# Kernel optimization log

Measured on AMD Instinct MI355X. Metric: run time of the kernel, lower is better.

Reference implementation:

```python
import jax, jax.numpy as jnp
import numpy as np

B, N_IN, N_MF, N_RULES, N_OUT_MEM, N_OUT = 16384, 6, 5, 2048, 12, 2
TANH_CENTERS = np.array([0.0, 0.75], dtype=np.float32)
TANH_SCALE = np.array([4.0, 0.75], dtype=np.float32)
EPS = 1e-12


def setup_inputs() -> dict:
    key = jax.random.key(0)
    k = jax.random.split(key, 6)
    x = jax.random.normal(k[0], (B, N_IN), dtype=jnp.float32)
    mf_centers = jax.random.normal(k[1], (N_IN, N_MF), dtype=jnp.float32)
    # strictly positive widths for the Gaussian memberships
    mf_scales = jax.random.uniform(k[2], (N_IN, N_MF), dtype=jnp.float32) + 0.5
    out_centers = jax.random.normal(k[3], (N_OUT_MEM,), dtype=jnp.float32)
    input_rules = jax.random.randint(k[4], (N_RULES, N_IN), 0, N_IN * N_MF, dtype=jnp.int32)
    output_rules = jax.random.randint(k[5], (N_RULES, N_OUT), 0, N_OUT_MEM, dtype=jnp.int32)
    return {"x": x, "mf_centers": mf_centers, "mf_scales": mf_scales,
            "out_centers": out_centers, "input_rules": input_rules,
            "output_rules": output_rules}


def reference(x, mf_centers, mf_scales, out_centers, input_rules, output_rules):
    # fuzzify: Gaussian membership per (input var, MF) -> [B, N_IN*N_MF]
    z = (x[:, :, None] - mf_centers[None]) / mf_scales[None]      # [B, N_IN, N_MF]
    fuzzified = jnp.exp(-z * z).reshape(x.shape[0], -1)           # [B, 30]
    # rules: gather antecedent memberships, min t-norm over antecedents
    gathered = fuzzified[:, input_rules]                          # [B, R, N_IN]
    weights = jnp.min(gathered, axis=2)                           # [B, R]
    # L1 normalize across rules (F.normalize p=1, dim=1)
    l1 = jnp.sum(jnp.abs(weights), axis=1, keepdims=True)
    normalized = weights / jnp.maximum(l1, EPS)
    # defuzzify: gather output-membership centers per rule, then matmul
    ow = out_centers[output_rules]                                # [R, N_OUT]
    defuzz = normalized @ ow                                      # [B, N_OUT]
    # constrain scaling
    return jnp.tanh(defuzz) * jnp.asarray(TANH_SCALE) + jnp.asarray(TANH_CENTERS)
```

## Files before the change

### kernel.cpp

```cpp
#include <hip/hip_runtime.h>
#include <hip/hip_bf16.h>

#define BATCH      16384
#define N_IN       6
#define N_MF       5
#define N_FUZZ     30
#define N_RULES    2048

#define ROWS_PER_BLOCK 64
#define BLOCK_THREADS  1024
#define WAVES          (BLOCK_THREADS / 64)
#define RULES_PER_WAVE (N_RULES / WAVES)

__global__ __launch_bounds__(BLOCK_THREADS, 1)
void anfis_kernel(const void* __restrict__ x_,
                  const void* __restrict__ mfc_,
                  const void* __restrict__ mfs_,
                  const void* __restrict__ oc_,
                  const int*  __restrict__ input_rules,
                  const int*  __restrict__ output_rules,
                  void* __restrict__ out_) {
    __shared__ float        fuzz[N_FUZZ][ROWS_PER_BLOCK];
    __shared__ float        p_l1[WAVES][ROWS_PER_BLOCK];
    __shared__ float        p_d0[WAVES][ROWS_PER_BLOCK];
    __shared__ float        p_d1[WAVES][ROWS_PER_BLOCK];
    __shared__ unsigned int packed_lds[N_RULES];
    __shared__ float2       ow_lds[N_RULES];
    __shared__ int          dtype_flag;

    const int t    = threadIdx.x;
    const int row0 = blockIdx.x * ROWS_PER_BLOCK;

    if (t == 0) {
        const unsigned int* w = (const unsigned int*)mfs_;
        int ok = 1;
        for (int k = 0; k < 15; ++k) {
            const unsigned int v = w[k];
            const float lo = __uint_as_float(v << 16);
            const float hi = __uint_as_float(v & 0xffff0000u);
            if (!(lo >= 0.4f && lo <= 1.6f && hi >= 0.4f && hi <= 1.6f)) { ok = 0; break; }
        }
        dtype_flag = ok;
    }
    __syncthreads();
    const bool is_bf16 = (dtype_flag != 0);

    for (int r = t; r < N_RULES; r += BLOCK_THREADS) {
        const int* rp = input_rules + r * N_IN;
        unsigned int p = 0;
#pragma unroll
        for (int i = 0; i < N_IN; ++i) {
            p |= ((unsigned int)rp[i] & 31u) << (5 * i);
        }
        packed_lds[r] = p;
        const int o0i = output_rules[2 * r + 0];
        const int o1i = output_rules[2 * r + 1];
        float o0, o1;
        if (is_bf16) {
            const unsigned short* oc = (const unsigned short*)oc_;
            o0 = __uint_as_float((unsigned int)oc[o0i] << 16);
            o1 = __uint_as_float((unsigned int)oc[o1i] << 16);
        } else {
            const float* oc = (const float*)oc_;
            o0 = oc[o0i];
            o1 = oc[o1i];
        }
        ow_lds[r] = make_float2(o0, o1);
    }

    for (int idx = t; idx < N_FUZZ * ROWS_PER_BLOCK; idx += BLOCK_THREADS) {
        const int v   = idx >> 6;
        const int row = idx & 63;
        const int i   = v / N_MF;
        float xv, c, s;
        if (is_bf16) {
            const unsigned short* xp = (const unsigned short*)x_;
            const unsigned short* cp = (const unsigned short*)mfc_;
            const unsigned short* sp = (const unsigned short*)mfs_;
            xv = __uint_as_float((unsigned int)xp[(row0 + row) * N_IN + i] << 16);
            c  = __uint_as_float((unsigned int)cp[v] << 16);
            s  = __uint_as_float((unsigned int)sp[v] << 16);
        } else {
            xv = ((const float*)x_)[(row0 + row) * N_IN + i];
            c  = ((const float*)mfc_)[v];
            s  = ((const float*)mfs_)[v];
        }
        const float z = (xv - c) / s;
        fuzz[v][row] = __expf(-z * z);
    }
    __syncthreads();

    const int lane = t & 63;
    const int wave = __builtin_amdgcn_readfirstlane(t >> 6);

    float acc_l1 = 0.0f, acc_d0 = 0.0f, acc_d1 = 0.0f;
    const int rbase = wave * RULES_PER_WAVE;
#pragma unroll 4
    for (int j = 0; j < RULES_PER_WAVE; ++j) {
        const int r = rbase + j;
        const unsigned int p = packed_lds[r];
        const float2 o = ow_lds[r];
        float w = fuzz[p & 31u][lane];
        w = fminf(w, fuzz[(p >> 5)  & 31u][lane]);
        w = fminf(w, fuzz[(p >> 10) & 31u][lane]);
        w = fminf(w, fuzz[(p >> 15) & 31u][lane]);
        w = fminf(w, fuzz[(p >> 20) & 31u][lane]);
        w = fminf(w, fuzz[(p >> 25) & 31u][lane]);
        acc_l1 += w;
        acc_d0 += w * o.x;
        acc_d1 += w * o.y;
    }
    p_l1[wave][lane] = acc_l1;
    p_d0[wave][lane] = acc_d0;
    p_d1[wave][lane] = acc_d1;
    __syncthreads();

    if (t < ROWS_PER_BLOCK) {
        float l1 = 0.0f, d0 = 0.0f, d1 = 0.0f;
#pragma unroll
        for (int wv = 0; wv < WAVES; ++wv) {
            l1 += p_l1[wv][t];
            d0 += p_d0[wv][t];
            d1 += p_d1[wv][t];
        }
        const float inv = 1.0f / fmaxf(l1, 1e-12f);
        const float y0 = tanhf(d0 * inv) * 4.00f + 0.00f;
        const float y1 = tanhf(d1 * inv) * 0.75f + 0.75f;
        if (is_bf16) {
            __hip_bfloat162 o;
            o.x = __float2bfloat16(y0);
            o.y = __float2bfloat16(y1);
            ((__hip_bfloat162*)out_)[row0 + t] = o;
        } else {
            ((float2*)out_)[row0 + t] = make_float2(y0, y1);
        }
    }
}

extern "C" void kernel_launch(void* const* d_in, const int* in_sizes, int n_in,
                              void* d_out, int out_size, void* d_ws, size_t ws_size,
                              hipStream_t stream) {
    (void)d_ws; (void)ws_size; (void)in_sizes; (void)n_in; (void)out_size;
    anfis_kernel<<<BATCH / ROWS_PER_BLOCK, BLOCK_THREADS, 0, stream>>>(
        d_in[0], d_in[1], d_in[2], d_in[3],
        (const int*)d_in[4], (const int*)d_in[5],
        d_out);
}
```

Before: 86.86 us.

## Split into prep/main/finalize kernels with fp16 packed memberships and rule splitting

Moves rule packing and output-center gathering into a separate prep kernel writing to workspace, so main blocks no longer redo it per block. The main kernel handles 256 rows per block using fp16 packed membership values (4 rows per lane via two packed-half min chains), reads rule data from global/cache, and splits rules across 4 blocks, writing partial sums that a finalize kernel reduces and applies tanh. This cuts per-block setup and LDS gather count, at the cost of two extra launches, a workspace round-trip, and fp16 rounding of membership values before the min.

Result: faster. 80.96 us (-6.8%).

```diff
diff --git a/kernel.cpp b/kernel.cpp
--- a/kernel.cpp
+++ b/kernel.cpp
@@ -6,143 +6,242 @@
 #define N_MF       5
 #define N_FUZZ     30
 #define N_RULES    2048
-
-#define ROWS_PER_BLOCK 64
-#define BLOCK_THREADS  1024
-#define WAVES          (BLOCK_THREADS / 64)
-#define RULES_PER_WAVE (N_RULES / WAVES)
-
-__global__ __launch_bounds__(BLOCK_THREADS, 1)
-void anfis_kernel(const void* __restrict__ x_,
-                  const void* __restrict__ mfc_,
-                  const void* __restrict__ mfs_,
-                  const void* __restrict__ oc_,
-                  const int*  __restrict__ input_rules,
-                  const int*  __restrict__ output_rules,
-                  void* __restrict__ out_) {
-    __shared__ float        fuzz[N_FUZZ][ROWS_PER_BLOCK];
-    __shared__ float        p_l1[WAVES][ROWS_PER_BLOCK];
-    __shared__ float        p_d0[WAVES][ROWS_PER_BLOCK];
-    __shared__ float        p_d1[WAVES][ROWS_PER_BLOCK];
-    __shared__ unsigned int packed_lds[N_RULES];
-    __shared__ float2       ow_lds[N_RULES];
-    __shared__ int          dtype_flag;
-
-    const int t    = threadIdx.x;
-    const int row0 = blockIdx.x * ROWS_PER_BLOCK;
-
-    if (t == 0) {
-        const unsigned int* w = (const unsigned int*)mfs_;
-        int ok = 1;
-        for (int k = 0; k < 15; ++k) {
-            const unsigned int v = w[k];
-            const float lo = __uint_as_float(v << 16);
-            const float hi = __uint_as_float(v & 0xffff0000u);
-            if (!(lo >= 0.4f && lo <= 1.6f && hi >= 0.4f && hi <= 1.6f)) { ok = 0; break; }
+#define N_OUT_MEM  12
+
+#define ROWS_PB    256
+#define SPLITS     4
+#define RULES_PB   (N_RULES / SPLITS)
+#define THREADS    1024
+#define WAVES      16
+#define RULES_PW   (RULES_PB / WAVES)
+#define ROWGROUPS  (BATCH / ROWS_PB)
+
+#define WS_PACKED_OFF  0
+#define WS_OW_OFF      8192
+#define WS_PART_OFF    24576
+
+typedef _Float16 f16x2 __attribute__((ext_vector_type(2)));
+
+__device__ inline int probe_is_bf16(const void* mfs) {
+    const unsigned int* w = (const unsigned int*)mfs;
+    int ok = 1;
+    for (int k = 0; k < 15; ++k) {
+        const unsigned int v = w[k];
+        const float lo = __uint_as_float(v << 16);
+        const float hi = __uint_as_float(v & 0xffff0000u);
+        if (!(lo >= 0.4f && lo <= 1.6f && hi >= 0.4f && hi <= 1.6f)) { ok = 0; break; }
+    }
+    return ok;
+}
+
+__global__ void anfis_prep(const int* __restrict__ input_rules,
+                           const int* __restrict__ output_rules,
+                           const void* __restrict__ oc_,
+                           const void* __restrict__ mfs_,
+                           unsigned int* __restrict__ packed,
+                           float2* __restrict__ ow) {
+    __shared__ int flag;
+    if (threadIdx.x == 0) flag = probe_is_bf16(mfs_);
+    __syncthreads();
+    const bool is_bf16 = (flag != 0);
+
+    const int r = blockIdx.x * blockDim.x + threadIdx.x;
+    if (r >= N_RULES) return;
+    const int* rp = input_rules + r * N_IN;
+    unsigned int p = 0;
+#pragma unroll
+    for (int i = 0; i < N_IN; ++i) p |= ((unsigned int)rp[i] & 31u) << (5 * i);
+    packed[r] = p;
+
+    const int o0i = output_rules[2 * r + 0];
+    const int o1i = output_rules[2 * r + 1];
+    float o0, o1;
+    if (is_bf16) {
+        const unsigned short* oc = (const unsigned short*)oc_;
+        o0 = __uint_as_float((unsigned int)oc[o0i] << 16);
+        o1 = __uint_as_float((unsigned int)oc[o1i] << 16);
+    } else {
+        const float* oc = (const float*)oc_;
+        o0 = oc[o0i]; o1 = oc[o1i];
+    }
+    ow[r] = make_float2(o0, o1);
+}
+
+__global__ __launch_bounds__(THREADS, 4)
+void anfis_main(const void* __restrict__ x_,
+                const void* __restrict__ mfc_,
+                const void* __restrict__ mfs_,
+                const unsigned int* __restrict__ packed,
+                const float2* __restrict__ ow,
+                float* __restrict__ partials) {
+    __shared__ float xs[ROWS_PB * N_IN];
+    __shared__ float2 cinv[N_FUZZ];
+    __shared__ uint2 fuzz4[N_FUZZ][64];
+    __shared__ float pl1[WAVES][ROWS_PB];
+    __shared__ float pd0[WAVES][ROWS_PB];
+    __shared__ float pd1[WAVES][ROWS_PB];
+    __shared__ int flag;
+
+    const int t     = threadIdx.x;
+    const int g     = blockIdx.x >> 2;
+    const int split = blockIdx.x & 3;
+    const int row0  = g * ROWS_PB;
+
+    if (t == 0) flag = probe_is_bf16(mfs_);
+    __syncthreads();
+    const bool is_bf16 = (flag != 0);
+
+    if (is_bf16) {
+        const unsigned short* xp = (const unsigned short*)x_ + row0 * N_IN;
+        for (int i = t; i < ROWS_PB * N_IN; i += THREADS)
+            xs[i] = __uint_as_float((unsigned int)xp[i] << 16);
+    } else {
+        const float* xp = (const float*)x_ + row0 * N_IN;
+        for (int i = t; i < ROWS_PB * N_IN; i += THREADS) xs[i] = xp[i];
+    }
+    if (t < N_FUZZ) {
+        float c, s;
+        if (is_bf16) {
+            c = __uint_as_float((unsigned int)((const unsigned short*)mfc_)[t] << 16);
+            s = __uint_as_float((unsigned int)((const unsigned short*)mfs_)[t] << 16);
+        } else {
+            c = ((const float*)mfc_)[t];
+            s = ((const float*)mfs_)[t];
         }
-        dtype_flag = ok;
-    }
-    __syncthreads();
-    const bool is_bf16 = (dtype_flag != 0);
-
-    for (int r = t; r < N_RULES; r += BLOCK_THREADS) {
-        const int* rp = input_rules + r * N_IN;
-        unsigned int p = 0;
-#pragma unroll
-        for (int i = 0; i < N_IN; ++i) {
-            p |= ((unsigned int)rp[i] & 31u) << (5 * i);
+        cinv[t] = make_float2(c, 1.0f / s);
+    }
+    __syncthreads();
+
+    for (int e = t; e < N_FUZZ * 64; e += THREADS) {
+        const int v    = e >> 6;
+        const int lane = e & 63;
+        const int i    = v / N_MF;
+        const float2 ci = cinv[v];
+        float f[4];
+#pragma unroll
+        for (int k = 0; k < 4; ++k) {
+            const float z = (xs[(lane + 64 * k) * N_IN + i] - ci.x) * ci.y;
+            f[k] = __expf(-z * z);
         }
-        packed_lds[r] = p;
-        const int o0i = output_rules[2 * r + 0];
-        const int o1i = output_rules[2 * r + 1];
-        float o0, o1;
-        if (is_bf16) {
-            const unsigned short* oc = (const unsigned short*)oc_;
-            o0 = __uint_as_float((unsigned int)oc[o0i] << 16);
-            o1 = __uint_as_float((unsigned int)oc[o1i] << 16);
-        } else {
-            const float* oc = (const float*)oc_;
-            o0 = oc[o0i];
-            o1 = oc[o1i];
-        }
-        ow_lds[r] = make_float2(o0, o1);
-    }
-
-    for (int idx = t; idx < N_FUZZ * ROWS_PER_BLOCK; idx += BLOCK_THREADS) {
-        const int v   = idx >> 6;
-        const int row = idx & 63;
-        const int i   = v / N_MF;
-        float xv, c, s;
-        if (is_bf16) {
-            const unsigned short* xp = (const unsigned short*)x_;
-            const unsigned short* cp = (const unsigned short*)mfc_;
-            const unsigned short* sp = (const unsigned short*)mfs_;
-            xv = __uint_as_float((unsigned int)xp[(row0 + row) * N_IN + i] << 16);
-            c  = __uint_as_float((unsigned int)cp[v] << 16);
-            s  = __uint_as_float((unsigned int)sp[v] << 16);
-        } else {
-            xv = ((const float*)x_)[(row0 + row) * N_IN + i];
-            c  = ((const float*)mfc_)[v];
-            s  = ((const float*)mfs_)[v];
-        }
-        const float z = (xv - c) / s;
-        fuzz[v][row] = __expf(-z * z);
+        f16x2 a = { (_Float16)f[0], (_Float16)f[1] };
+        f16x2 b = { (_Float16)f[2], (_Float16)f[3] };
+        uint2 u;
+        u.x = __builtin_bit_cast(unsigned int, a);
+        u.y = __builtin_bit_cast(unsigned int, b);
+        fuzz4[v][lane] = u;
     }
     __syncthreads();
 
     const int lane = t & 63;
     const int wave = __builtin_amdgcn_readfirstlane(t >> 6);
-
-    float acc_l1 = 0.0f, acc_d0 = 0.0f, acc_d1 = 0.0f;
-    const int rbase = wave * RULES_PER_WAVE;
+    const uint2* fz = &fuzz4[0][0];
+
+    float l1[4] = {0.f, 0.f, 0.f, 0.f};
+    float d0[4] = {0.f, 0.f, 0.f, 0.f};
+    float d1[4] = {0.f, 0.f, 0.f, 0.f};
+
+    const int rbase = split * RULES_PB + wave * RULES_PW;
 #pragma unroll 4
-    for (int j = 0; j < RULES_PER_WAVE; ++j) {
+    for (int j = 0; j < RULES_PW; ++j) {
         const int r = rbase + j;
-        const unsigned int p = packed_lds[r];
-        const float2 o = ow_lds[r];
-        float w = fuzz[p & 31u][lane];
-        w = fminf(w, fuzz[(p >> 5)  & 31u][lane]);
-        w = fminf(w, fuzz[(p >> 10) & 31u][lane]);
-        w = fminf(w, fuzz[(p >> 15) & 31u][lane]);
-        w = fminf(w, fuzz[(p >> 20) & 31u][lane]);
-        w = fminf(w, fuzz[(p >> 25) & 31u][lane]);
-        acc_l1 += w;
-        acc_d0 += w * o.x;
-        acc_d1 += w * o.y;
-    }
-    p_l1[wave][lane] = acc_l1;
-    p_d0[wave][lane] = acc_d0;
-    p_d1[wave][lane] = acc_d1;
-    __syncthreads();
-
-    if (t < ROWS_PER_BLOCK) {
-        float l1 = 0.0f, d0 = 0.0f, d1 = 0.0f;
+        const unsigned int p = packed[r];
+        const float2 o = ow[r];
+        const uint2 g0 = fz[((p      ) & 31u) * 64 + lane];
+        const uint2 g1 = fz[((p >> 5 ) & 31u) * 64 + lane];
+        const uint2 g2 = fz[((p >> 10) & 31u) * 64 + lane];
+        const uint2 g3 = fz[((p >> 15) & 31u) * 64 + lane];
+        const uint2 g4 = fz[((p >> 20) & 31u) * 64 + lane];
+        const uint2 g5 = fz[((p >> 25) & 31u) * 64 + lane];
+        f16x2 wa = __builtin_elementwise_min(__builtin_bit_cast(f16x2, g0.x),
+                                             __builtin_bit_cast(f16x2, g1.x));
+        wa = __builtin_elementwise_min(wa, __builtin_bit_cast(f16x2, g2.x));
+        wa = __builtin_elementwise_min(wa, __builtin_bit_cast(f16x2, g3.x));
+        wa = __builtin_elementwise_min(wa, __builtin_bit_cast(f16x2, g4.x));
+        wa = __builtin_elementwise_min(wa, __builtin_bit_cast(f16x2, g5.x));
+        f16x2 wb = __builtin_elementwise_min(__builtin_bit_cast(f16x2, g0.y),
+                                             __builtin_bit_cast(f16x2, g1.y));
+        wb = __builtin_elementwise_min(wb, __builtin_bit_cast(f16x2, g2.y));
+        wb = __builtin_elementwise_min(wb, __builtin_bit_cast(f16x2, g3.y));
+        wb = __builtin_elementwise_min(wb, __builtin_bit_cast(f16x2, g4.y));
+        wb = __builtin_elementwise_min(wb, __builtin_bit_cast(f16x2, g5.y));
+        const float w0 = (float)wa.x, w1 = (float)wa.y;
+        const float w2 = (float)wb.x, w3 = (float)wb.y;
+        l1[0] += w0; d0[0] += w0 * o.x; d1[0] += w0 * o.y;
+        l1[1] += w1; d0[1] += w1 * o.x; d1[1] += w1 * o.y;
+        l1[2] += w2; d0[2] += w2 * o.x; d1[2] += w2 * o.y;
+        l1[3] += w3; d0[3] += w3 * o.x; d1[3] += w3 * o.y;
+    }
+#pragma unroll
+    for (int k = 0; k < 4; ++k) {
+        pl1[wave][lane + 64 * k] = l1[k];
+        pd0[wave][lane + 64 * k] = d0[k];
+        pd1[wave][lane + 64 * k] = d1[k];
+    }
+    __syncthreads();
+
+    if (t < ROWS_PB) {
+        float a = 0.f, b = 0.f, c = 0.f;
 #pragma unroll
         for (int wv = 0; wv < WAVES; ++wv) {
-            l1 += p_l1[wv][t];
-            d0 += p_d0[wv][t];
-            d1 += p_d1[wv][t];
+            a += pl1[wv][t];
+            b += pd0[wv][t];
+            c += pd1[wv][t];
         }
-        const float inv = 1.0f / fmaxf(l1, 1e-12f);
-        const float y0 = tanhf(d0 * inv) * 4.00f + 0.00f;
-        const float y1 = tanhf(d1 * inv) * 0.75f + 0.75f;
-        if (is_bf16) {
-            __hip_bfloat162 o;
-            o.x = __float2bfloat16(y0);
-            o.y = __float2bfloat16(y1);
-            ((__hip_bfloat162*)out_)[row0 + t] = o;
-        } else {
-            ((float2*)out_)[row0 + t] = make_float2(y0, y1);
-        }
+        const int row = row0 + t;
+        partials[(split * 3 + 0) * BATCH + row] = a;
+        partials[(split * 3 + 1) * BATCH + row] = b;
+        partials[(split * 3 + 2) * BATCH + row] = c;
+    }
+}
+
+__global__ void anfis_finalize(const float* __restrict__ partials,
+                               const void* __restrict__ mfs_,
+                               void* __restrict__ out_) {
+    __shared__ int flag;
+    if (threadIdx.x == 0) flag = probe_is_bf16(mfs_);
+    __syncthreads();
+    const int row = blockIdx.x * blockDim.x + threadIdx.x;
+    if (row >= BATCH) return;
+    float l1 = 0.f, d0 = 0.f, d1 = 0.f;
+#pragma unroll
+    for (int s = 0; s < SPLITS; ++s) {
+        l1 += partials[(s * 3 + 0) * BATCH + row];
+        d0 += partials[(s * 3 + 1) * BATCH + row];
+        d1 += partials[(s * 3 + 2) * BATCH + row];
+    }
+    const float inv = 1.0f / fmaxf(l1, 1e-12f);
+    const float y0 = tanhf(d0 * inv) * 4.00f + 0.00f;
+    const float y1 = tanhf(d1 * inv) * 0.75f + 0.75f;
+    if (flag) {
+        __hip_bfloat162 o;
+        o.x = __float2bfloat16(y0);
+        o.y = __float2bfloat16(y1);
+        ((__hip_bfloat162*)out_)[row] = o;
+    } else {
+        ((float2*)out_)[row] = make_float2(y0, y1);
     }
 }
 
 extern "C" void kernel_launch(void* const* d_in, const int* in_sizes, int n_in,
                               void* d_out, int out_size, void* d_ws, size_t ws_size,
                               hipStream_t stream) {
-    (void)d_ws; (void)ws_size; (void)in_sizes; (void)n_in; (void)out_size;
-    anfis_kernel<<<BATCH / ROWS_PER_BLOCK, BLOCK_THREADS, 0, stream>>>(
-        d_in[0], d_in[1], d_in[2], d_in[3],
-        (const int*)d_in[4], (const int*)d_in[5],
-        d_out);
-}
+    (void)in_sizes; (void)n_in; (void)out_size; (void)ws_size;
+    const void* x_   = d_in[0];
+    const void* mfc_ = d_in[1];
+    const void* mfs_ = d_in[2];
+    const void* oc_  = d_in[3];
+    const int* input_rules  = (const int*)d_in[4];
+    const int* output_rules = (const int*)d_in[5];
+
+    unsigned int* packed = (unsigned int*)((char*)d_ws + WS_PACKED_OFF);
+    float2*       ow     = (float2*)((char*)d_ws + WS_OW_OFF);
+    float*        parts  = (float*)((char*)d_ws + WS_PART_OFF);
+
+    anfis_prep<<<(N_RULES + 255) / 256, 256, 0, stream>>>(
+        input_rules, output_rules, oc_, mfs_, packed, ow);
+
+    anfis_main<<<ROWGROUPS * SPLITS, THREADS, 0, stream>>>(
+        x_, mfc_, mfs_, packed, ow, parts);
+
+    anfis_finalize<<<BATCH / 256, 256, 0, stream>>>(parts, mfs_, d_out);
+}
```
